# Kernel tuning notes

Measured on AMD Instinct MI355X. Metric: run time of the kernel, lower is better.

Reference implementation:

```python
import jax, jax.numpy as jnp
import numpy as np
import math

B, H, W, CV = 8, 128, 128, 256
T, CT = 77, 512
HEADS, HEAD_DIM = 8, 32
TOP_M = 5
LN_EPS = 1e-5
NORM_EPS = 1e-6
CLAMP = 2.0


def _ln(x, w, b):
    mu = jnp.mean(x, axis=-1, keepdims=True)
    var = jnp.mean(jnp.square(x - mu), axis=-1, keepdims=True)
    return (x - mu) * jax.lax.rsqrt(var + LN_EPS) * w + b


def _l2norm(x):
    n = jnp.sqrt(jnp.sum(jnp.square(x), axis=-1, keepdims=True))
    return x / jnp.maximum(n, NORM_EPS)


def setup_inputs() -> dict:
    key = jax.random.key(0)
    ks = jax.random.split(key, 12)
    s = 0.02
    return {
        "visual_features": jax.random.normal(ks[0], (B, H, W, CV), jnp.float32),
        "text_features": jax.random.normal(ks[1], (B, T, CT), jnp.float32),
        "norm1_w": jnp.ones((CV,), jnp.float32),
        "norm1_b": jnp.zeros((CV,), jnp.float32),
        "q_w": s * jax.random.normal(ks[2], (CV, CV), jnp.float32),
        "q_b": jnp.zeros((CV,), jnp.float32),
        "k_w": s * jax.random.normal(ks[3], (CT, CV), jnp.float32),
        "k_b": jnp.zeros((CV,), jnp.float32),
        "v_w": s * jax.random.normal(ks[4], (CT, CV), jnp.float32),
        "v_b": jnp.zeros((CV,), jnp.float32),
        "out_w": s * jax.random.normal(ks[5], (CV, CV), jnp.float32),
        "out_b": jnp.zeros((CV,), jnp.float32),
        "gate_w": s * jax.random.normal(ks[6], (CV, 1), jnp.float32),
        "gate_b": jnp.zeros((1,), jnp.float32),
        "logit_scale": jnp.asarray(math.log(1.0 / 0.07), jnp.float32),
        "alpha": jnp.asarray(0.1, jnp.float32),
        "norm2_w": jnp.ones((CV,), jnp.float32),
        "norm2_b": jnp.zeros((CV,), jnp.float32),
        "ffn1_w": s * jax.random.normal(ks[7], (CV, 4 * CV), jnp.float32),
        "ffn1_b": jnp.zeros((4 * CV,), jnp.float32),
        "ffn2_w": s * jax.random.normal(ks[8], (4 * CV, CV), jnp.float32),
        "ffn2_b": jnp.zeros((CV,), jnp.float32),
    }


def reference(visual_features, text_features, norm1_w, norm1_b, q_w, q_b, k_w, k_b,
              v_w, v_b, out_w, out_b, gate_w, gate_b, logit_scale, alpha,
              norm2_w, norm2_b, ffn1_w, ffn1_b, ffn2_w, ffn2_b):
    b, h, w, cv = visual_features.shape
    n = h * w
    # Pre-LN then flatten spatial dims: (B, N, Cv)
    x = _ln(visual_features, norm1_w, norm1_b).reshape(b, n, cv)
    q_full = x @ q_w + q_b                      # (B, N, Cv)
    k_full = text_features @ k_w + k_b          # (B, T, Cv)
    v_full = text_features @ v_w + v_b          # (B, T, Cv)
    # padding mask: all-zero text tokens
    pad = jnp.sum(jnp.abs(text_features), axis=-1) <= 1e-6  # (B, T)
    # cosine-normalize over FULL Cv dim, then split heads
    q = _l2norm(q_full).reshape(b, n, HEADS, HEAD_DIM)
    k = _l2norm(k_full).reshape(b, -1, HEADS, HEAD_DIM)
    v = v_full.reshape(b, -1, HEADS, HEAD_DIM)
    scale = jnp.exp(jnp.clip(logit_scale, -CLAMP, CLAMP)) / jnp.sqrt(jnp.float32(HEAD_DIM))
    sim = jnp.einsum('bnhd,bthd->bnht', q, k) * scale  # (B, N, Hh, T)
    sim = jnp.where(pad[:, None, None, :], -jnp.inf, sim)
    # top-k pruning over text tokens (threshold at k-th value; ties measure-zero)
    topv = jax.lax.top_k(sim, TOP_M)[0]
    sim = jnp.where(sim >= topv[..., -1:], sim, -jnp.inf)
    attn = jax.nn.softmax(sim, axis=-1)
    aligned = jnp.einsum('bnht,bthd->bnhd', attn, v).reshape(b, n, cv)
    aligned = aligned @ out_w + out_b
    gate = jax.nn.sigmoid(x @ gate_w + gate_b)  # (B, N, 1)
    y = x + alpha * gate * aligned
    y = _ln(y, norm2_w, norm2_b)
    ffn = jax.nn.gelu(y @ ffn1_w + ffn1_b, approximate=False) @ ffn2_w + ffn2_b
    y = y + ffn
    return y.reshape(b, h, w, cv)
```

## Files before the change

kernel.cpp:

```cpp
#include <hip/hip_runtime.h>
#include <hip/hip_bf16.h>

typedef _Float16 h16;
typedef __attribute__((ext_vector_type(8))) _Float16 halfx8;
typedef __attribute__((ext_vector_type(4))) _Float16 halfx4;
typedef __attribute__((ext_vector_type(4))) float f32x4;

__device__ __forceinline__ void gload_lds16(const void* g, void* l) {
  __builtin_amdgcn_global_load_lds((const __attribute__((address_space(1))) unsigned int*)g,
                                   (__attribute__((address_space(3))) unsigned int*)l, 16, 0, 0);
}
__device__ __forceinline__ unsigned umax_(unsigned a, unsigned b) { return a > b ? a : b; }
__device__ __forceinline__ unsigned umin_(unsigned a, unsigned b) { return a < b ? a : b; }

__device__ __forceinline__ float fast_gelu(float v) {
  float x2 = v * v;
  float w_ = v * fmaf(x2, 0.0713548163f, 1.5957691216f);
  float e = __expf(w_);
  float r = 1.f / (1.f + e);
  return v * e * r;
}

__global__ __launch_bounds__(256) void prep_kernel(
    const float* __restrict__ tf, const float* __restrict__ kw, const float* __restrict__ kb,
    const float* __restrict__ vw, const float* __restrict__ vb, const float* __restrict__ lsp,
    h16* __restrict__ ko, h16* __restrict__ vo, float* __restrict__ padf,
    const float* __restrict__ qw, const float* __restrict__ ow,
    const float* __restrict__ f1w, const float* __restrict__ f2w,
    h16* __restrict__ qwT, h16* __restrict__ owT,
    h16* __restrict__ f1T, h16* __restrict__ f2T,
    const float* __restrict__ vis, const float* __restrict__ n1w, const float* __restrict__ n1b,
    const float* __restrict__ gw, const float* __restrict__ gb,
    h16* __restrict__ x, float* __restrict__ gate)
{
  __shared__ h16 st[4 * 512];
  __shared__ float kro[4 * 256];
  __shared__ float ssc[4];
  int bid = blockIdx.x, tid = threadIdx.x;
  int lane = tid & 63, wid = tid >> 6;

  if (bid < 160) {
    int b = bid / 20, tg = bid % 20, t0 = tg * 4;
    for (int i = tid; i < 4 * 512; i += 256) {
      int tl = i >> 9, j = i & 511, t = t0 + tl;
      float v = (t < 77) ? tf[((size_t)b * 77 + t) * 512 + j] : 0.f;
      st[i] = (h16)v;
    }
    __syncthreads();
    {
      int t = t0 + wid;
      float a = 0.f;
      #pragma unroll
      for (int j = 0; j < 8; j++) a += fabsf((float)st[wid * 512 + lane + j * 64]);
      #pragma unroll
      for (int o = 32; o; o >>= 1) a += __shfl_xor(a, o);
      if (lane == 0) padf[b * 80 + t] = (a <= 1e-6f) ? -1e30f : 0.f;
    }
    int c = tid;
    float kacc[4], vacc[4];
    #pragma unroll
    for (int tl = 0; tl < 4; tl++) { kacc[tl] = kb[c]; vacc[tl] = vb[c]; }
    for (int j = 0; j < 512; j++) {
      float wkv = kw[(size_t)j * 256 + c];
      float wvv = vw[(size_t)j * 256 + c];
      #pragma unroll
      for (int tl = 0; tl < 4; tl++) {
        float xv = (float)st[tl * 512 + j];
        kacc[tl] += xv * wkv; vacc[tl] += xv * wvv;
      }
    }
    #pragma unroll
    for (int tl = 0; tl < 4; tl++) kro[tl * 256 + c] = kacc[tl] * kacc[tl];
    __syncthreads();
    {
      float s2 = kro[wid * 256 + lane] + kro[wid * 256 + lane + 64]
               + kro[wid * 256 + lane + 128] + kro[wid * 256 + lane + 192];
      #pragma unroll
      for (int o = 32; o; o >>= 1) s2 += __shfl_xor(s2, o);
      if (lane == 0) {
        float ls = lsp[0];
        float scale = __expf(fminf(fmaxf(ls, -2.f), 2.f)) * rsqrtf(32.f);
        ssc[wid] = scale / fmaxf(sqrtf(s2), 1e-6f);
      }
    }
    __syncthreads();
    int h = c >> 5, d = c & 31, g = d >> 3, e = d & 7;
    #pragma unroll
    for (int tl = 0; tl < 4; tl++) {
      int t = t0 + tl;
      int kt = t >> 4, l15 = t & 15, ln = g * 16 + l15;
      size_t koff = ((((size_t)(b * 8 + h) * 5 + kt) * 64) + ln) * 8 + e;
      size_t voff = (((size_t)(b * 8 + h) * 80) + t) * 32 + d;
      ko[koff] = (t < 77) ? (h16)(kacc[tl] * ssc[tl]) : (h16)0.f;
      vo[voff] = (t < 77) ? (h16)vacc[tl] : (h16)0.f;
    }
  } else if (bid < 2720) {
    int cb = bid - 160;
    const float* in; h16* out; int logN, K, base;
    if (cb < 256)       { in = qw;  out = qwT; logN = 8;  K = 256;  base = 0; }
    else if (cb < 512)  { in = ow;  out = owT; logN = 8;  K = 256;  base = 256; }
    else if (cb < 1536) { in = f1w; out = f1T; logN = 10; K = 256;  base = 512; }
    else                { in = f2w; out = f2T; logN = 8;  K = 1024; base = 1536; }
    int idx = (cb - base) * 256 + tid;
    int k = idx >> logN, n = idx & ((1 << logN) - 1);
    out[(size_t)n * K + k] = (h16)in[idx];
  } else {
    size_t row = (size_t)(bid - 2720) * 4 + wid;
    const float4 v = ((const float4*)(vis + row * 256))[lane];
    float s = v.x + v.y + v.z + v.w;
    float q = v.x * v.x + v.y * v.y + v.z * v.z + v.w * v.w;
    #pragma unroll
    for (int o = 32; o; o >>= 1) { s += __shfl_xor(s, o); q += __shfl_xor(q, o); }
    float mean = s * (1.f / 256.f);
    float rstd = rsqrtf(q * (1.f / 256.f) - mean * mean + 1e-5f);
    float4 wv = ((const float4*)n1w)[lane], bv = ((const float4*)n1b)[lane];
    float x0 = (v.x - mean) * rstd * wv.x + bv.x;
    float x1 = (v.y - mean) * rstd * wv.y + bv.y;
    float x2 = (v.z - mean) * rstd * wv.z + bv.z;
    float x3 = (v.w - mean) * rstd * wv.w + bv.w;
    float4 gv = ((const float4*)gw)[lane];
    float g = x0 * gv.x + x1 * gv.y + x2 * gv.z + x3 * gv.w;
    #pragma unroll
    for (int o = 32; o; o >>= 1) g += __shfl_xor(g, o);
    if (lane == 0) gate[row] = 1.f / (1.f + __expf(-(g + gb[0])));
    halfx4 o4; o4[0] = (h16)x0; o4[1] = (h16)x1; o4[2] = (h16)x2; o4[3] = (h16)x3;
    ((halfx4*)(x + row * 256))[lane] = o4;
  }
}

__global__ __launch_bounds__(256) void gemmQA_kernel(const h16* __restrict__ A,
    const h16* __restrict__ Wt, const float* __restrict__ bias,
    const h16* __restrict__ kk,
    const h16* __restrict__ vv,
    const float* __restrict__ padf,
    h16* __restrict__ outp)
{
  __shared__ char sA[8192];
  __shared__ char sB[32768];
  int m0 = blockIdx.x * 64;
  int tid = threadIdx.x, lane = tid & 63, wid = tid >> 6;
  int wn = wid;
  int l15 = lane & 15, l4 = lane >> 4, xk = l15 & 7;
  f32x4 acc[4][4];
  #pragma unroll
  for (int a = 0; a < 4; a++)
    #pragma unroll
    for (int b2 = 0; b2 < 4; b2++) acc[a][b2] = (f32x4){0.f, 0.f, 0.f, 0.f};
  const size_t sa = 512;
  int srow = lane >> 3;
  int scol = ((lane & 7) ^ srow) * 16;
  const char* Ab = (const char*)A + (size_t)m0 * sa + scol;
  const char* Bb = (const char*)Wt + scol;
  for (int k0 = 0; k0 < 256; k0 += 64) {
    #pragma unroll
    for (int cc = 0; cc < 2; cc++) {
      int ch = wid * 2 + cc;
      gload_lds16(Ab + (size_t)(ch * 8 + srow) * sa + k0 * 2, sA + ch * 1024);
    }
    #pragma unroll
    for (int cc = 0; cc < 8; cc++) {
      int ch = wid * 8 + cc;
      gload_lds16(Bb + (size_t)(ch * 8 + srow) * sa + k0 * 2, sB + ch * 1024);
    }
    asm volatile("s_waitcnt vmcnt(0)" ::: "memory");
    __syncthreads();
    #pragma unroll
    for (int ks = 0; ks < 2; ks++) {
      halfx8 af[4], bf[4];
      #pragma unroll
      for (int f = 0; f < 4; f++) {
        af[f] = *(const halfx8*)(sA + (f * 16 + l15) * 128 + (((ks * 4 + l4) ^ xk) * 16));
        bf[f] = *(const halfx8*)(sB + (wn * 64 + f * 16 + l15) * 128 + (((ks * 4 + l4) ^ xk) * 16));
      }
      #pragma unroll
      for (int fm = 0; fm < 4; fm++)
        #pragma unroll
        for (int fn = 0; fn < 4; fn++)
          acc[fm][fn] = __builtin_amdgcn_mfma_f32_16x16x32_f16(af[fm], bf[fn], acc[fm][fn], 0, 0, 0);
    }
    __syncthreads();
  }
  float bv[4];
  #pragma unroll
  for (int fn = 0; fn < 4; fn++) bv[fn] = bias[wn * 64 + fn * 16 + l15];
  float ps[4][4];
  #pragma unroll
  for (int fm = 0; fm < 4; fm++)
    #pragma unroll
    for (int r = 0; r < 4; r++) {
      float s = 0.f;
      #pragma unroll
      for (int fn = 0; fn < 4; fn++) {
        float v = acc[fm][fn][r] + bv[fn];
        acc[fm][fn][r] = v;
        s += v * v;
      }
      ps[fm][r] = s;
    }
  #pragma unroll
  for (int o = 1; o <= 8; o <<= 1)
    #pragma unroll
    for (int fm = 0; fm < 4; fm++)
      #pragma unroll
      for (int r = 0; r < 4; r++) ps[fm][r] += __shfl_xor(ps[fm][r], o);
  if (l15 == 0) {
    #pragma unroll
    for (int fm = 0; fm < 4; fm++)
      #pragma unroll
      for (int r = 0; r < 4; r++)
        ((float*)sA)[(fm * 16 + l4 * 4 + r) * 4 + wn] = ps[fm][r];
  }
  __syncthreads();
  #pragma unroll
  for (int fm = 0; fm < 4; fm++)
    #pragma unroll
    for (int r = 0; r < 4; r++) {
      const float* p = (const float*)sA + (fm * 16 + l4 * 4 + r) * 4;
      float S = p[0] + p[1] + p[2] + p[3];
      float sc = 1.f / fmaxf(sqrtf(S), 1e-6f);
      int row = fm * 16 + l4 * 4 + r;
      #pragma unroll
      for (int fn = 0; fn < 4; fn++) {
        int col = wn * 64 + fn * 16 + l15;
        ((h16*)(sB + row * 512 + (((col >> 3) ^ (row & 7)) * 16)))[col & 7] =
            (h16)(acc[fm][fn][r] * sc);
      }
    }
  __syncthreads();

  {
    int bx = blockIdx.x;
    int g = l4;
    int b = bx >> 8;
    size_t qrow = (size_t)bx * 64 + wid * 16 + l15;
    int base4 = g * 4;
    float pad4[5][4];
    #pragma unroll
    for (int kt = 0; kt < 5; kt++) {
      float4 p4 = *(const float4*)&padf[b * 80 + kt * 16 + base4];
      pad4[kt][0] = p4.x; pad4[kt][1] = p4.y; pad4[kt][2] = p4.z; pad4[kt][3] = p4.w;
    }
    const char* qsrc = sB + (wid * 16 + l15) * 512;
    int rk = l15 & 7;
    h16* op = &outp[qrow * 256 + g * 8];
    #pragma unroll 2
    for (int h = 0; h < 8; h++) {
      int ho = h * 32;
      halfx8 qf = *(const halfx8*)(qsrc + (((h * 4 + l4) ^ rk) * 16));
      const h16* kph = kk + (((size_t)(b * 8 + h) * 5) * 64 + lane) * 8;
      const h16* vph = vv + ((size_t)(b * 8 + h) * 80) * 32 + g * 8;
      f32x4 acc5[5];
      #pragma unroll
      for (int kt = 0; kt < 5; kt++) {
        halfx8 kf = *(const halfx8*)(kph + kt * 512);
        acc5[kt] = __builtin_amdgcn_mfma_f32_16x16x32_f16(kf, qf, (f32x4){0.f, 0.f, 0.f, 0.f}, 0, 0, 0);
      }
      unsigned pv0 = 0u, pv1 = 0u, pv2 = 0u, pv3 = 0u, pv4 = 0u;
      #pragma unroll
      for (int kt = 0; kt < 5; kt++) {
        #pragma unroll
        for (int r = 0; r < 4; r++) {
          float s = acc5[kt][r] + pad4[kt][r];
          int bi = __float_as_int(s);
          unsigned u = ((unsigned)(bi ^ ((bi >> 31) | (int)0x80000000)) & 0xFFFFFF80u)
                     | (unsigned)(base4 + kt * 16 + r);
          unsigned a;
          a = umax_(pv0, u); u = umin_(pv0, u); pv0 = a;
          a = umax_(pv1, u); u = umin_(pv1, u); pv1 = a;
          a = umax_(pv2, u); u = umin_(pv2, u); pv2 = a;
          a = umax_(pv3, u); u = umin_(pv3, u); pv3 = a;
          pv4 = umax_(pv4, u);
        }
      }
      #pragma unroll
      for (int mrd = 0; mrd < 2; mrd++) {
        int msk = mrd ? 32 : 16;
        unsigned b0 = (unsigned)__shfl_xor((int)pv0, msk);
        unsigned b1 = (unsigned)__shfl_xor((int)pv1, msk);
        unsigned b2 = (unsigned)__shfl_xor((int)pv2, msk);
        unsigned b3 = (unsigned)__shfl_xor((int)pv3, msk);
        unsigned b4 = (unsigned)__shfl_xor((int)pv4, msk);
        unsigned c0 = umax_(pv0, b0);
        unsigned c1 = umax_(umax_(umin_(pv0, b0), pv1), b1);
        unsigned c2 = umax_(umax_(umin_(pv0, b1), umin_(pv1, b0)), umax_(pv2, b2));
        unsigned c3 = umax_(umax_(umax_(umin_(pv0, b2), umin_(pv1, b1)), umin_(pv2, b0)), umax_(pv3, b3));
        unsigned c4 = umax_(umax_(umax_(umin_(pv0, b3), umin_(pv1, b2)),
                                  umax_(umin_(pv2, b1), umin_(pv3, b0))), umax_(pv4, b4));
        pv0 = c0; pv1 = c1; pv2 = c2; pv3 = c3; pv4 = c4;
      }
      unsigned pvs[5] = {pv0, pv1, pv2, pv3, pv4};
      float pw[5]; int ti[5]; float den = 0.f;
      #pragma unroll
      for (int k = 0; k < 5; k++) {
        unsigned u = pvs[k];
        int sg = ((int)u) >> 31;
        float tv = __int_as_float(u ^ (0x80000000u | (unsigned)~sg));
        ti[k] = (int)(u & 0x7Fu);
        pw[k] = __expf(tv);
        den += pw[k];
      }
      float inv = 1.f / den;
      halfx8 o8 = {};
      #pragma unroll
      for (int k = 0; k < 5; k++) {
        h16 ph = (h16)(pw[k] * inv);
        halfx8 v = *(const halfx8*)(vph + ti[k] * 32);
        halfx8 p8 = {ph, ph, ph, ph, ph, ph, ph, ph};
        o8 = o8 + p8 * v;
      }
      *(halfx8*)(op + ho) = o8;
    }
  }
}

__global__ __launch_bounds__(256) void gemmO_kernel(const h16* __restrict__ A,
    const h16* __restrict__ Wt, const float* __restrict__ ob,
    const h16* __restrict__ x, const float* __restrict__ gate,
    const float* __restrict__ alphap, const float* __restrict__ w2,
    const float* __restrict__ b2, h16* __restrict__ outp)
{
  __shared__ char sA[8192];
  __shared__ char sB[32768];
  int m0 = blockIdx.x * 64;
  int tid = threadIdx.x, lane = tid & 63, wid = tid >> 6;
  int wn = wid;
  int l15 = lane & 15, l4 = lane >> 4, xk = l15 & 7;
  f32x4 acc[4][4];
  #pragma unroll
  for (int a = 0; a < 4; a++)
    #pragma unroll
    for (int b2_ = 0; b2_ < 4; b2_++) acc[a][b2_] = (f32x4){0.f, 0.f, 0.f, 0.f};
  const size_t sa = 512;
  int srow = lane >> 3;
  int scol = ((lane & 7) ^ srow) * 16;
  const char* Ab = (const char*)A + (size_t)m0 * sa + scol;
  const char* Bb = (const char*)Wt + scol;
  for (int k0 = 0; k0 < 256; k0 += 64) {
    #pragma unroll
    for (int cc = 0; cc < 2; cc++) {
      int ch = wid * 2 + cc;
      gload_lds16(Ab + (size_t)(ch * 8 + srow) * sa + k0 * 2, sA + ch * 1024);
    }
    #pragma unroll
    for (int cc = 0; cc < 8; cc++) {
      int ch = wid * 8 + cc;
      gload_lds16(Bb + (size_t)(ch * 8 + srow) * sa + k0 * 2, sB + ch * 1024);
    }
    asm volatile("s_waitcnt vmcnt(0)" ::: "memory");
    __syncthreads();
    #pragma unroll
    for (int ks = 0; ks < 2; ks++) {
      halfx8 af[4], bf[4];
      #pragma unroll
      for (int f = 0; f < 4; f++) {
        af[f] = *(const halfx8*)(sA + (f * 16 + l15) * 128 + (((ks * 4 + l4) ^ xk) * 16));
        bf[f] = *(const halfx8*)(sB + (wn * 64 + f * 16 + l15) * 128 + (((ks * 4 + l4) ^ xk) * 16));
      }
      #pragma unroll
      for (int fm = 0; fm < 4; fm++)
        #pragma unroll
        for (int fn = 0; fn < 4; fn++)
          acc[fm][fn] = __builtin_amdgcn_mfma_f32_16x16x32_f16(af[fm], bf[fn], acc[fm][fn], 0, 0, 0);
    }
    __syncthreads();
  }
  float bv[4], w2v[4], b2v[4];
  #pragma unroll
  for (int fn = 0; fn < 4; fn++) {
    int col = wn * 64 + fn * 16 + l15;
    bv[fn] = ob[col]; w2v[fn] = w2[col]; b2v[fn] = b2[col];
  }
  float al = alphap[0];
  float s1[4][4], s2[4][4];
  #pragma unroll
  for (int fm = 0; fm < 4; fm++)
    #pragma unroll
    for (int r = 0; r < 4; r++) {
      size_t row = (size_t)(m0 + fm * 16 + l4 * 4 + r);
      float ga = al * gate[row];
      float a1 = 0.f, a2 = 0.f;
      #pragma unroll
      for (int fn = 0; fn < 4; fn++) {
        float v = acc[fm][fn][r] + bv[fn];
        float xv = (float)x[row * 256 + wn * 64 + fn * 16 + l15];
        float y = xv + ga * v;
        acc[fm][fn][r] = y;
        a1 += y; a2 += y * y;
      }
      s1[fm][r] = a1; s2[fm][r] = a2;
    }
  #pragma unroll
  for (int o = 1; o <= 8; o <<= 1)
    #pragma unroll
    for (int fm = 0; fm < 4; fm++)
      #pragma unroll
      for (int r = 0; r < 4; r++) {
        s1[fm][r] += __shfl_xor(s1[fm][r], o);
        s2[fm][r] += __shfl_xor(s2[fm][r], o);
      }
  if (l15 == 0) {
    #pragma unroll
    for (int fm = 0; fm < 4; fm++)
      #pragma unroll
      for (int r = 0; r < 4; r++) {
        int rr = fm * 16 + l4 * 4 + r;
        ((float*)sA)[rr * 8 + wn * 2 + 0] = s1[fm][r];
        ((float*)sA)[rr * 8 + wn * 2 + 1] = s2[fm][r];
      }
  }
  __syncthreads();
  #pragma unroll
  for (int fm = 0; fm < 4; fm++)
    #pragma unroll
    for (int r = 0; r < 4; r++) {
      int rr = fm * 16 + l4 * 4 + r;
      const float* p = (const float*)sA + rr * 8;
      float S1 = p[0] + p[2] + p[4] + p[6];
      float S2 = p[1] + p[3] + p[5] + p[7];
      float mean = S1 * (1.f / 256.f);
      float var = S2 * (1.f / 256.f) - mean * mean;
      float rstd = rsqrtf(var + 1e-5f);
      size_t row = (size_t)(m0 + rr);
      #pragma unroll
      for (int fn = 0; fn < 4; fn++) {
        float y = acc[fm][fn][r];
        outp[row * 256 + wn * 64 + fn * 16 + l15] =
            (h16)((y - mean) * rstd * w2v[fn] + b2v[fn]);
      }
    }
}

__device__ __forceinline__ void ffn_stage_w1(const h16* __restrict__ w1t,
                                             int c, char* dW1, int tid, int wid)
{
  #pragma unroll
  for (int j = 0; j < 4; j++) {
    int i = j * 512 + tid;
    int r = i >> 5, g = i & 31;
    gload_lds16(w1t + (size_t)(c * 64 + r) * 256 + ((g ^ (r & 7)) * 8),
                dW1 + (j * 512 + wid * 64) * 16);
  }
}
__device__ __forceinline__ void ffn_stage_w2(const h16* __restrict__ w2t,
                                             int c, char* dW2, int tid, int wid)
{
  #pragma unroll
  for (int j = 0; j < 4; j++) {
    int i = j * 512 + tid;
    int r = i >> 3, g = i & 7;
    gload_lds16(w2t + (size_t)r * 1024 + c * 64 + ((g ^ (r & 7)) * 8),
                dW2 + (j * 512 + wid * 64) * 16);
  }
}

__global__ __launch_bounds__(512, 2) void ffn_fused_kernel(
    const h16* __restrict__ y2g, const h16* __restrict__ w1t, const float* __restrict__ b1,
    const h16* __restrict__ w2t, const float* __restrict__ b2, float* __restrict__ outp)
{
  __shared__ char smem[163840];
  float* sE = (float*)smem;

  int m0 = blockIdx.x * 128;
  int tid = threadIdx.x, lane = tid & 63, wid = tid >> 6;
  int l15 = lane & 15, l4 = lane >> 4;
  int wm1 = wid >> 1, wn1 = wid & 1;
  int wm2 = wid >> 2, wn2 = wid & 3;

  halfx8 afy[2][8];
  #pragma unroll
  for (int fm = 0; fm < 2; fm++) {
    size_t row = (size_t)(m0 + wm1 * 32 + fm * 16 + l15);
    #pragma unroll
    for (int ks = 0; ks < 8; ks++)
      afy[fm][ks] = *(const halfx8*)&y2g[row * 256 + ks * 32 + l4 * 8];
  }

  f32x4 acc2[4][4];
  #pragma unroll
  for (int a = 0; a < 4; a++)
    #pragma unroll
    for (int b_ = 0; b_ < 4; b_++) acc2[a][b_] = (f32x4){0.f, 0.f, 0.f, 0.f};

  ffn_stage_w1(w1t, 0, smem, tid, wid);
  float b1v0 = b1[wn1 * 32 + l15];
  float b1v1 = b1[wn1 * 32 + 16 + l15];
  asm volatile("s_waitcnt vmcnt(0)" ::: "memory");
  __builtin_amdgcn_s_barrier();
  asm volatile("" ::: "memory");

  for (int c = 0; c < 16; c++) {
    int buf = c & 1;
    char* sW1c = smem + buf * 32768;
    if (c < 15) ffn_stage_w1(w1t, c + 1, smem + (buf ^ 1) * 32768, tid, wid);
    ffn_stage_w2(w2t, c, smem + 65536 + buf * 32768, tid, wid);
    float nb0 = 0.f, nb1 = 0.f;
    if (c < 15) {
      nb0 = b1[(c + 1) * 64 + wn1 * 32 + l15];
      nb1 = b1[(c + 1) * 64 + wn1 * 32 + 16 + l15];
    }

    f32x4 a1[2][2];
    #pragma unroll
    for (int a = 0; a < 2; a++)
      #pragma unroll
      for (int b_ = 0; b_ < 2; b_++) a1[a][b_] = (f32x4){0.f, 0.f, 0.f, 0.f};
    __builtin_amdgcn_s_setprio(1);
    #pragma unroll
    for (int ks = 0; ks < 8; ks++) {
      #pragma unroll
      for (int fc = 0; fc < 2; fc++) {
        int nrow = wn1 * 32 + fc * 16 + l15;
        halfx8 bf = *(const halfx8*)(sW1c + (size_t)nrow * 512 + (((ks * 4 + l4) ^ (nrow & 7)) * 16));
        #pragma unroll
        for (int fm = 0; fm < 2; fm++)
          a1[fm][fc] = __builtin_amdgcn_mfma_f32_16x16x32_f16(afy[fm][ks], bf, a1[fm][fc], 0, 0, 0);
      }
    }
    __builtin_amdgcn_s_setprio(0);

    {
      char* sHc = smem + 131072 + buf * 16384;
      #pragma unroll
      for (int fm = 0; fm < 2; fm++)
        #pragma unroll
        for (int fc = 0; fc < 2; fc++)
          #pragma unroll
          for (int r = 0; r < 4; r++) {
            int row = wm1 * 32 + fm * 16 + l4 * 4 + r;
            int col = wn1 * 32 + fc * 16 + l15;
            float v = fast_gelu(a1[fm][fc][r] + (fc ? b1v1 : b1v0));
            ((h16*)(sHc + row * 128 + (((col >> 3) ^ (row & 7)) * 16)))[col & 7] = (h16)v;
          }
    }

    if (c > 0) {
      char* sHp = smem + 131072 + (buf ^ 1) * 16384;
      char* sW2p = smem + 65536 + (buf ^ 1) * 32768;
      __builtin_amdgcn_s_setprio(1);
      #pragma unroll
      for (int ks = 0; ks < 2; ks++) {
        halfx8 ah[4], bw[4];
        #pragma unroll
        for (int f = 0; f < 4; f++) {
          int hrow = wm2 * 64 + f * 16 + l15;
          ah[f] = *(const halfx8*)(sHp + hrow * 128 + (((ks * 4 + l4) ^ (hrow & 7)) * 16));
          int wrow = wn2 * 64 + f * 16 + l15;
          bw[f] = *(const halfx8*)(sW2p + (size_t)wrow * 128 + (((ks * 4 + l4) ^ (wrow & 7)) * 16));
        }
        #pragma unroll
        for (int fm = 0; fm < 4; fm++)
          #pragma unroll
          for (int fn = 0; fn < 4; fn++)
            acc2[fm][fn] = __builtin_amdgcn_mfma_f32_16x16x32_f16(ah[fm], bw[fn], acc2[fm][fn], 0, 0, 0);
      }
      __builtin_amdgcn_s_setprio(0);
    }

    asm volatile("s_waitcnt lgkmcnt(0)" ::: "memory");
    asm volatile("s_waitcnt vmcnt(0)" ::: "memory");
    __builtin_amdgcn_s_barrier();
    asm volatile("" ::: "memory");
    b1v0 = nb0; b1v1 = nb1;
  }

  {
    char* sHp = smem + 131072 + 16384;
    char* sW2p = smem + 65536 + 32768;
    __builtin_amdgcn_s_setprio(1);
    #pragma unroll
    for (int ks = 0; ks < 2; ks++) {
      halfx8 ah[4], bw[4];
      #pragma unroll
      for (int f = 0; f < 4; f++) {
        int hrow = wm2 * 64 + f * 16 + l15;
        ah[f] = *(const halfx8*)(sHp + hrow * 128 + (((ks * 4 + l4) ^ (hrow & 7)) * 16));
        int wrow = wn2 * 64 + f * 16 + l15;
        bw[f] = *(const halfx8*)(sW2p + (size_t)wrow * 128 + (((ks * 4 + l4) ^ (wrow & 7)) * 16));
      }
      #pragma unroll
      for (int fm = 0; fm < 4; fm++)
        #pragma unroll
        for (int fn = 0; fn < 4; fn++)
          acc2[fm][fn] = __builtin_amdgcn_mfma_f32_16x16x32_f16(ah[fm], bw[fn], acc2[fm][fn], 0, 0, 0);
    }
    __builtin_amdgcn_s_setprio(0);
  }

  int rowl = tid >> 3, cg = tid & 7;
  #pragma unroll
  for (int half = 0; half < 2; half++) {
    if (wm2 == half) {
      #pragma unroll
      for (int fm = 0; fm < 4; fm++)
        #pragma unroll
        for (int fn = 0; fn < 4; fn++)
          #pragma unroll
          for (int r = 0; r < 4; r++)
            sE[(fm * 16 + l4 * 4 + r) * 264 + wn2 * 64 + fn * 16 + l15] = acc2[fm][fn][r];
    }
    __syncthreads();
    size_t grow = (size_t)(m0 + half * 64 + rowl);
    #pragma unroll
    for (int k = 0; k < 8; k++) {
      int c0 = cg * 4 + k * 32;
      float4 v = *(float4*)&sE[rowl * 264 + c0];
      halfx4 rv = *(const halfx4*)&y2g[grow * 256 + c0];
      float4 bb = *(const float4*)&b2[c0];
      float4 o;
      o.x = v.x + (float)rv[0] + bb.x;
      o.y = v.y + (float)rv[1] + bb.y;
      o.z = v.z + (float)rv[2] + bb.z;
      o.w = v.w + (float)rv[3] + bb.w;
      *(float4*)&outp[grow * 256 + c0] = o;
    }
    __syncthreads();
  }
}

extern "C" void kernel_launch(void* const* d_in, const int* in_sizes, int n_in,
                              void* d_out, int out_size, void* d_ws, size_t ws_size,
                              hipStream_t stream)
{
  const float* vis = (const float*)d_in[0];
  const float* tf  = (const float*)d_in[1];
  const float* n1w = (const float*)d_in[2];
  const float* n1b = (const float*)d_in[3];
  const float* qw  = (const float*)d_in[4];
  const float* qb  = (const float*)d_in[5];
  const float* kw  = (const float*)d_in[6];
  const float* kb  = (const float*)d_in[7];
  const float* vw  = (const float*)d_in[8];
  const float* vb  = (const float*)d_in[9];
  const float* ow  = (const float*)d_in[10];
  const float* ob  = (const float*)d_in[11];
  const float* gw  = (const float*)d_in[12];
  const float* gb  = (const float*)d_in[13];
  const float* ls  = (const float*)d_in[14];
  const float* al  = (const float*)d_in[15];
  const float* n2w = (const float*)d_in[16];
  const float* n2b = (const float*)d_in[17];
  const float* f1w = (const float*)d_in[18];
  const float* f1b = (const float*)d_in[19];
  const float* f2w = (const float*)d_in[20];
  const float* f2b = (const float*)d_in[21];

  char* ws = (char*)d_ws;
  const size_t MB_ = 1024ull * 1024ull;
  h16*  kS   = (h16*)(ws + 0 * MB_);
  h16*  vS   = (h16*)(ws + 1 * MB_);
  float* padf = (float*)(ws + 2 * MB_);
  float* gate = (float*)(ws + 3 * MB_);
  h16*  qwT  = (h16*)(ws + 4 * MB_);
  h16*  owT  = (h16*)(ws + 5 * MB_);
  h16*  f1T  = (h16*)(ws + 6 * MB_);
  h16*  f2T  = (h16*)(ws + 7 * MB_);
  h16*  xh   = (h16*)(ws + 16 * MB_);
  h16*  qh   = (h16*)(ws + 80 * MB_);
  h16*  alg  = (h16*)(ws + 144 * MB_);

  prep_kernel<<<35488, 256, 0, stream>>>(
      tf, kw, kb, vw, vb, ls, kS, vS, padf,
      qw, ow, f1w, f2w, qwT, owT, f1T, f2T,
      vis, n1w, n1b, gw, gb, xh, gate);

  gemmQA_kernel<<<2048, 256, 0, stream>>>(xh, qwT, qb, kS, vS, padf, qh);

  gemmO_kernel<<<2048, 256, 0, stream>>>(qh, owT, ob, xh, gate, al, n2w, n2b, alg);

  ffn_fused_kernel<<<1024, 512, 0, stream>>>(alg, f1T, f1b, f2T, f2b, (float*)d_out);
}
```

Measured before the change: 489.1 us.

## Load FFN2 weight fragments directly into registers instead of staging through LDS

The second FFN GEMM's weight chunks were previously copied into a double-buffered LDS region and then read back. Each wave now loads its own W2 fragments straight from global memory into registers, prefetching the next chunk after the current MFMAs. This removes 64KB of LDS traffic and staging, shrinking shared memory from 160KB to 96KB. In exchange, W2 is re-read from global/L2 by every wave with no LDS sharing, and register pressure rises; launch bounds change to 1 block per CU min.

```diff
diff --git a/kernel.cpp b/kernel.cpp
--- a/kernel.cpp
+++ b/kernel.cpp
@@ -441,23 +441,12 @@
                 dW1 + (j * 512 + wid * 64) * 16);
   }
 }
-__device__ __forceinline__ void ffn_stage_w2(const h16* __restrict__ w2t,
-                                             int c, char* dW2, int tid, int wid)
-{
-  #pragma unroll
-  for (int j = 0; j < 4; j++) {
-    int i = j * 512 + tid;
-    int r = i >> 3, g = i & 7;
-    gload_lds16(w2t + (size_t)r * 1024 + c * 64 + ((g ^ (r & 7)) * 8),
-                dW2 + (j * 512 + wid * 64) * 16);
-  }
-}
-
-__global__ __launch_bounds__(512, 2) void ffn_fused_kernel(
+
+__global__ __launch_bounds__(512, 1) void ffn_fused_kernel(
     const h16* __restrict__ y2g, const h16* __restrict__ w1t, const float* __restrict__ b1,
     const h16* __restrict__ w2t, const float* __restrict__ b2, float* __restrict__ outp)
 {
-  __shared__ char smem[163840];
+  __shared__ char smem[98304];
   float* sE = (float*)smem;
 
   int m0 = blockIdx.x * 128;
@@ -481,7 +470,15 @@
     #pragma unroll
     for (int b_ = 0; b_ < 4; b_++) acc2[a][b_] = (f32x4){0.f, 0.f, 0.f, 0.f};
 
+  const h16* w2base = w2t + (size_t)(wn2 * 64 + l15) * 1024 + l4 * 8;
+  halfx8 bw[2][4];
+
   ffn_stage_w1(w1t, 0, smem, tid, wid);
+  #pragma unroll
+  for (int ks = 0; ks < 2; ks++)
+    #pragma unroll
+    for (int f = 0; f < 4; f++)
+      bw[ks][f] = *(const halfx8*)(w2base + (size_t)(f * 16) * 1024 + ks * 32);
   float b1v0 = b1[wn1 * 32 + l15];
   float b1v1 = b1[wn1 * 32 + 16 + l15];
   asm volatile("s_waitcnt vmcnt(0)" ::: "memory");
@@ -492,7 +489,6 @@
     int buf = c & 1;
     char* sW1c = smem + buf * 32768;
     if (c < 15) ffn_stage_w1(w1t, c + 1, smem + (buf ^ 1) * 32768, tid, wid);
-    ffn_stage_w2(w2t, c, smem + 65536 + buf * 32768, tid, wid);
     float nb0 = 0.f, nb1 = 0.f;
     if (c < 15) {
       nb0 = b1[(c + 1) * 64 + wn1 * 32 + l15];
@@ -519,7 +515,7 @@
     __builtin_amdgcn_s_setprio(0);
 
     {
-      char* sHc = smem + 131072 + buf * 16384;
+      char* sHc = smem + 65536 + buf * 16384;
       #pragma unroll
       for (int fm = 0; fm < 2; fm++)
         #pragma unroll
@@ -534,26 +530,28 @@
     }
 
     if (c > 0) {
-      char* sHp = smem + 131072 + (buf ^ 1) * 16384;
-      char* sW2p = smem + 65536 + (buf ^ 1) * 32768;
+      char* sHp = smem + 65536 + (buf ^ 1) * 16384;
       __builtin_amdgcn_s_setprio(1);
       #pragma unroll
       for (int ks = 0; ks < 2; ks++) {
-        halfx8 ah[4], bw[4];
+        halfx8 ah[4];
         #pragma unroll
         for (int f = 0; f < 4; f++) {
           int hrow = wm2 * 64 + f * 16 + l15;
           ah[f] = *(const halfx8*)(sHp + hrow * 128 + (((ks * 4 + l4) ^ (hrow & 7)) * 16));
-          int wrow = wn2 * 64 + f * 16 + l15;
-          bw[f] = *(const halfx8*)(sW2p + (size_t)wrow * 128 + (((ks * 4 + l4) ^ (wrow & 7)) * 16));
         }
         #pragma unroll
         for (int fm = 0; fm < 4; fm++)
           #pragma unroll
           for (int fn = 0; fn < 4; fn++)
-            acc2[fm][fn] = __builtin_amdgcn_mfma_f32_16x16x32_f16(ah[fm], bw[fn], acc2[fm][fn], 0, 0, 0);
+            acc2[fm][fn] = __builtin_amdgcn_mfma_f32_16x16x32_f16(ah[fm], bw[ks][fn], acc2[fm][fn], 0, 0, 0);
       }
       __builtin_amdgcn_s_setprio(0);
+      #pragma unroll
+      for (int ks = 0; ks < 2; ks++)
+        #pragma unroll
+        for (int f = 0; f < 4; f++)
+          bw[ks][f] = *(const halfx8*)(w2base + (size_t)(f * 16) * 1024 + c * 64 + ks * 32);
     }
 
     asm volatile("s_waitcnt lgkmcnt(0)" ::: "memory");
@@ -564,24 +562,21 @@
   }
 
   {
-    char* sHp = smem + 131072 + 16384;
-    char* sW2p = smem + 65536 + 32768;
+    char* sHp = smem + 65536 + 16384;
     __builtin_amdgcn_s_setprio(1);
     #pragma unroll
     for (int ks = 0; ks < 2; ks++) {
-      halfx8 ah[4], bw[4];
+      halfx8 ah[4];
       #pragma unroll
       for (int f = 0; f < 4; f++) {
         int hrow = wm2 * 64 + f * 16 + l15;
         ah[f] = *(const halfx8*)(sHp + hrow * 128 + (((ks * 4 + l4) ^ (hrow & 7)) * 16));
-        int wrow = wn2 * 64 + f * 16 + l15;
-        bw[f] = *(const halfx8*)(sW2p + (size_t)wrow * 128 + (((ks * 4 + l4) ^ (wrow & 7)) * 16));
       }
       #pragma unroll
       for (int fm = 0; fm < 4; fm++)
         #pragma unroll
         for (int fn = 0; fn < 4; fn++)
-          acc2[fm][fn] = __builtin_amdgcn_mfma_f32_16x16x32_f16(ah[fm], bw[fn], acc2[fm][fn], 0, 0, 0);
+          acc2[fm][fn] = __builtin_amdgcn_mfma_f32_16x16x32_f16(ah[fm], bw[ks][fn], acc2[fm][fn], 0, 0, 0);
     }
     __builtin_amdgcn_s_setprio(0);
   }
```

Measured after the change: 553.1 us. 13.1% more time.
